# Optimization experiments

Hardware: AMD Instinct MI355X
Metric: run time of the kernel (lower is better)

## Reference

```python
import jax, jax.numpy as jnp
import numpy as np

GRID_DIMS = (64, 64, 64)
GRID_LOWER = np.array([0.0, 0.0, 0.0], np.float32)
GRID_STEPS = np.array([0.015625, 0.015625, 0.015625], np.float32)
RADIUS = 0.03125
STENCIL = 2  # ceil(radius / step)


def _poly6(d2, h):
    # standard SPH poly6 smoothing kernel: 315/(64 pi h^9) (h^2 - d^2)^3, d <= h
    c = np.float32(315.0 / (64.0 * np.pi * h ** 9))
    return jnp.where(d2 <= h * h, c * (h * h - d2) ** 3, 0.0)


def particles2grid(locs, data, density):
    # locs [B,N,3], data [B,N,C], density [B,N] -> grid [B,X,Y,Z,C]
    B, N, _ = locs.shape
    C = data.shape[-1]
    X, Y, Z = GRID_DIMS
    dims = jnp.array(GRID_DIMS, jnp.int32)
    r = jnp.arange(-STENCIL, STENCIL + 1)
    offs = jnp.stack(jnp.meshgrid(r, r, r, indexing='ij'), -1).reshape(-1, 3)  # [K,3]
    base = jnp.floor((locs - GRID_LOWER) / GRID_STEPS).astype(jnp.int32)        # [B,N,3]
    cells = base[:, :, None, :] + offs                                          # [B,N,K,3]
    centers = GRID_LOWER + (cells.astype(locs.dtype) + 0.5) * GRID_STEPS
    d2 = jnp.sum((centers - locs[:, :, None, :]) ** 2, -1)                      # [B,N,K]
    w = _poly6(d2, RADIUS)
    w = jnp.where(jnp.all((cells >= 0) & (cells < dims), -1), w, 0.0)
    contrib = w[..., None] * (data / density[..., None])[:, :, None, :]         # [B,N,K,C]
    cells = jnp.clip(cells, 0, dims - 1)
    flat = (cells[..., 0] * Y + cells[..., 1]) * Z + cells[..., 2]              # [B,N,K]

    def splat(f, c):
        return jnp.zeros((X * Y * Z, C), data.dtype).at[f.reshape(-1)].add(c.reshape(-1, C))

    return jax.vmap(splat)(flat, contrib).reshape(B, X, Y, Z, C)


def grid2particles(grid, locs):
    # trilinear interpolation of grid [B,X,Y,Z,C] at particle locations [B,N,3]
    B, X, Y, Z, C = grid.shape
    dims = jnp.array([X, Y, Z], jnp.int32)
    pos = (locs - GRID_LOWER) / GRID_STEPS - 0.5                                # cell-center coords
    i0 = jnp.floor(pos).astype(jnp.int32)
    frac = pos - i0.astype(locs.dtype)
    gflat = grid.reshape(B, X * Y * Z, C)
    gather = jax.vmap(lambda g, f: g[f])                                        # [B,N] -> [B,N,C]
    out = jnp.zeros((B, locs.shape[1], C), grid.dtype)
    for dx in (0, 1):
        for dy in (0, 1):
            for dz in (0, 1):
                off = jnp.array([dx, dy, dz], jnp.int32)
                idx = i0 + off
                wd = jnp.where(off == 1, frac, 1.0 - frac)                      # [B,N,3]
                w = wd[..., 0] * wd[..., 1] * wd[..., 2]
                w = jnp.where(jnp.all((idx >= 0) & (idx < dims), -1), w, 0.0)
                idx = jnp.clip(idx, 0, dims - 1)
                flat = (idx[..., 0] * Y + idx[..., 1]) * Z + idx[..., 2]
                out = out + w[..., None] * gather(gflat, flat)
    return out


def conv3d(x, w, b):
    y = jax.lax.conv_general_dilated(x, w, (1, 1, 1), 'SAME',
                                     dimension_numbers=('NCDHW', 'OIDHW', 'NCDHW'))
    return y + b[None, :, None, None, None]


def prelu(x, a):
    return jnp.where(x >= 0, x, a * x)


def setup_inputs() -> dict:
    key = jax.random.key(0)
    ks = jax.random.split(key, 8)
    B, N = 2, 32768
    Cin, K, Cout = 4, 32, 4
    s = lambda fan: np.float32(1.0 / np.sqrt(fan * 27))
    return {
        'locs': jax.random.uniform(ks[0], (B, N, 3), jnp.float32),
        'data': jax.random.normal(ks[1], (B, N, Cin), jnp.float32),
        'density': jax.random.uniform(ks[2], (B, N), jnp.float32, 0.5, 1.5),
        'W0': jax.random.normal(ks[3], (K, Cin, 3, 3, 3), jnp.float32) * s(Cin),
        'b0': jnp.zeros((K,), jnp.float32),
        'W1': jax.random.normal(ks[4], (K, K, 3, 3, 3), jnp.float32) * s(K),
        'b1': jnp.zeros((K,), jnp.float32),
        'W2': jax.random.normal(ks[5], (K, K, 3, 3, 3), jnp.float32) * s(K),
        'b2': jnp.zeros((K,), jnp.float32),
        'W3': jax.random.normal(ks[6], (Cout, K, 3, 3, 3), jnp.float32) * s(K),
        'b3': jnp.zeros((Cout,), jnp.float32),
        'a0': jnp.full((1,), 0.25, jnp.float32),
        'a1': jnp.full((1,), 0.25, jnp.float32),
        'a2': jnp.full((1,), 0.25, jnp.float32),
    }


def reference(locs, data, density, W0, b0, W1, b1, W2, b2, W3, b3, a0, a1, a2):
    grid = particles2grid(locs, data, density)            # [B,X,Y,Z,Cin]
    g = jnp.transpose(grid, (0, 4, 1, 2, 3))              # NCDHW
    g = prelu(conv3d(g, W0, b0), a0)
    g = prelu(conv3d(g, W1, b1), a1)
    g = prelu(conv3d(g, W2, b2), a2)
    g = conv3d(g, W3, b3)
    g = jnp.transpose(g, (0, 2, 3, 4, 1))                 # [B,X,Y,Z,Cout]
    return grid2particles(g, locs)                        # [B,N,Cout]
```

## Files before the change

kernel.cpp:

```cpp
#include <hip/hip_runtime.h>

#define BATCH 2
#define NPART 32768
#define GD 64
#define NVOX (BATCH * GD * GD * GD)

typedef unsigned short ushortT;
typedef __attribute__((ext_vector_type(8))) short short8;
typedef __attribute__((ext_vector_type(16))) float float16;

__device__ __forceinline__ float poly6_c() {
    const double H9 = 1.0 / 35184372088832.0;
    return (float)(315.0 / (64.0 * 3.14159265358979323846 * H9));
}

__device__ __forceinline__ ushortT bf16_rne(float f) {
    unsigned int u = __float_as_uint(f);
    u = (u + 0x7fffu + ((u >> 16) & 1u)) >> 16;
    return (ushortT)u;
}

__device__ __forceinline__ int imax(int a, int b) { return a > b ? a : b; }
__device__ __forceinline__ int imin(int a, int b) { return a < b ? a : b; }

__global__ void zero_ints_kernel(int* __restrict__ p, int n) {
    int t = blockIdx.x * blockDim.x + threadIdx.x;
    if (t < n) p[t] = 0;
}

__global__ void zero_borders_kernel(ushortT* __restrict__ g8,
                                    ushortT* __restrict__ gA,
                                    ushortT* __restrict__ gB) {
    int t = blockIdx.x * 256 + threadIdx.x;
    if (t >= 147456) return;
    ushortT* base; int idx;
    if (t < 16384)      { base = g8; idx = t; }
    else if (t < 81920) { base = gA; idx = t - 16384; }
    else                { base = gB; idx = t - 81920; }
    int slot = (idx & 1) * 65; idx >>= 1;
    short8 z8 = {0, 0, 0, 0, 0, 0, 0, 0};
    *(short8*)(base + ((size_t)idx * 66 + slot) * 8) = z8;
}

__global__ __launch_bounds__(256) void bin_count_kernel(
    const float* __restrict__ locs, int* __restrict__ counts) {
    int t = blockIdx.x * blockDim.x + threadIdx.x;
    if (t >= BATCH * NPART) return;
    int b = t >> 15;
    int bx = ((int)floorf(locs[t * 3 + 0] * 64.0f)) >> 1;
    int by = ((int)floorf(locs[t * 3 + 1] * 64.0f)) >> 1;
    int bz = ((int)floorf(locs[t * 3 + 2] * 64.0f)) >> 1;
    atomicAdd(&counts[b * 32768 + ((bx * 32) + by) * 32 + bz], 1);
}

__global__ __launch_bounds__(256) void scanA_kernel(
    const int* __restrict__ counts, int* __restrict__ offsets,
    int* __restrict__ blockSum) {
    __shared__ int sh[256];
    int tid = threadIdx.x, g = blockIdx.x;
    int v = counts[g * 256 + tid];
    sh[tid] = v;
    __syncthreads();
    for (int off = 1; off < 256; off <<= 1) {
        int u = (tid >= off) ? sh[tid - off] : 0;
        __syncthreads();
        sh[tid] += u;
        __syncthreads();
    }
    offsets[g * 256 + tid] = sh[tid] - v;
    if (tid == 255) blockSum[g] = sh[255];
}

__global__ __launch_bounds__(256) void scanB_kernel(
    int* __restrict__ offsets, const int* __restrict__ blockSum) {
    __shared__ int sh[256];
    int tid = threadIdx.x, g = blockIdx.x;
    sh[tid] = (tid < g) ? blockSum[tid] : 0;
    __syncthreads();
    for (int off = 128; off > 0; off >>= 1) {
        if (tid < off) sh[tid] += sh[tid + off];
        __syncthreads();
    }
    offsets[g * 256 + tid] += sh[0];
    if (g == 255 && tid == 255) offsets[65536] = BATCH * NPART;
}

__global__ __launch_bounds__(256) void bin_scatter_kernel(
    const float* __restrict__ locs, const float* __restrict__ data,
    const float* __restrict__ density, const int* __restrict__ offsets,
    int* __restrict__ cursor, float* __restrict__ payload) {
    int t = blockIdx.x * blockDim.x + threadIdx.x;
    if (t >= BATCH * NPART) return;
    int b = t >> 15;
    float px = locs[t * 3 + 0];
    float py = locs[t * 3 + 1];
    float pz = locs[t * 3 + 2];
    int bx = ((int)floorf(px * 64.0f)) >> 1;
    int by = ((int)floorf(py * 64.0f)) >> 1;
    int bz = ((int)floorf(pz * 64.0f)) >> 1;
    int bb = b * 32768 + ((bx * 32) + by) * 32 + bz;
    int slot = atomicAdd(&cursor[bb], 1);
    int idx = offsets[bb] + slot;
    float inv_d = 1.0f / density[t];
    float4 p0 = {px, py, pz, data[t * 4 + 0] * inv_d};
    float4 p1 = {data[t * 4 + 1] * inv_d, data[t * 4 + 2] * inv_d,
                 data[t * 4 + 3] * inv_d, 0.f};
    *(float4*)(payload + idx * 8)     = p0;
    *(float4*)(payload + idx * 8 + 4) = p1;
}

__global__ __launch_bounds__(256) void splat_gather_kernel(
    const float* __restrict__ payload, const int* __restrict__ offsets,
    ushortT* __restrict__ g8) {
    __shared__ float plist[256 * 8];
    __shared__ int segS[36];
    __shared__ int segP[37];
    __shared__ int shTot[1];

    int wg = blockIdx.x;
    int sb = wg & 511, b = wg >> 9;
    int X0 = (sb >> 6) * 8, Y0 = ((sb >> 3) & 7) * 8, Z0 = (sb & 7) * 8;
    int tid = threadIdx.x;

    int bxlo = imax(0, (X0 - 2) >> 1), bxhi = imin(31, (X0 + 9) >> 1);
    int bylo = imax(0, (Y0 - 2) >> 1), byhi = imin(31, (Y0 + 9) >> 1);
    int bzlo = imax(0, (Z0 - 2) >> 1), bzhi = imin(31, (Z0 + 9) >> 1);
    int ny = byhi - bylo + 1;
    int ns = (bxhi - bxlo + 1) * ny;
    if (tid < ns) {
        int bx = bxlo + tid / ny, by = bylo + tid % ny;
        int row = b * 32768 + (bx * 32 + by) * 32;
        int s = offsets[row + bzlo];
        int e = offsets[row + bzhi + 1];
        segS[tid] = s;
        segP[tid] = e - s;
    }
    __syncthreads();
    if (tid == 0) {
        int p = 0;
        for (int k = 0; k < ns; ++k) { int len = segP[k]; segP[k] = p; p += len; }
        segP[ns] = p;
        shTot[0] = p;
    }
    __syncthreads();

    const float step = 0.015625f;
    const float h2 = 0.03125f * 0.03125f;
    const float cc = poly6_c();
    int total = shTot[0];

    int l = tid & 63, w = tid >> 6;
    int cx = X0 + 4 * (w >> 1) + (l >> 4);
    int cy = Y0 + 4 * (w & 1) + ((l >> 2) & 3);
    int cz0 = Z0 + (l & 3);
    float xc  = ((float)cx  + 0.5f) * step;
    float yc  = ((float)cy  + 0.5f) * step;
    float zc0 = ((float)cz0 + 0.5f) * step;
    float zc1 = zc0 + 4.0f * step;

    float a00 = 0.f, a01 = 0.f, a02 = 0.f, a03 = 0.f;
    float a10 = 0.f, a11 = 0.f, a12 = 0.f, a13 = 0.f;

    int nchunks = (total + 255) >> 8;
    for (int ch = 0; ch < nchunks; ++ch) {
        __syncthreads();
        int jj = (ch << 8) + tid;
        if (jj < total) {
            int k = 0;
            while (jj >= segP[k + 1]) ++k;
            int idx = segS[k] + (jj - segP[k]);
            *(float4*)(plist + tid * 8)     = *(const float4*)(payload + idx * 8);
            *(float4*)(plist + tid * 8 + 4) = *(const float4*)(payload + idx * 8 + 4);
        }
        __syncthreads();
        int cnt = imin(256, total - (ch << 8));
        for (int p = 0; p < cnt; ++p) {
            float4 pa = *(const float4*)(plist + p * 8);
            float dx = pa.x - xc, dy = pa.y - yc;
            float dxy2 = fmaf(dy, dy, dx * dx);
            if (!__any(dxy2 <= h2)) continue;
            float4 pv = *(const float4*)(plist + p * 8 + 4);
            float dz0 = pa.z - zc0;
            float d20 = fmaf(dz0, dz0, dxy2);
            float u0 = fmaxf(h2 - d20, 0.f);
            float w0 = (cc * u0) * (u0 * u0);
            a00 = fmaf(w0, pa.w, a00);
            a01 = fmaf(w0, pv.x, a01);
            a02 = fmaf(w0, pv.y, a02);
            a03 = fmaf(w0, pv.z, a03);
            float dz1 = pa.z - zc1;
            float d21 = fmaf(dz1, dz1, dxy2);
            float u1 = fmaxf(h2 - d21, 0.f);
            float w1 = (cc * u1) * (u1 * u1);
            a10 = fmaf(w1, pa.w, a10);
            a11 = fmaf(w1, pv.x, a11);
            a12 = fmaf(w1, pv.y, a12);
            a13 = fmaf(w1, pv.z, a13);
        }
    }

    size_t colIdx = (size_t)(((b * 64 + cx) * 64) + cy);
    short8 o;
    o[0] = (short)bf16_rne(a00); o[1] = (short)bf16_rne(a01);
    o[2] = (short)bf16_rne(a02); o[3] = (short)bf16_rne(a03);
    o[4] = 0; o[5] = 0; o[6] = 0; o[7] = 0;
    *(short8*)(g8 + (colIdx * 66 + (cz0 + 1)) * 8) = o;
    o[0] = (short)bf16_rne(a10); o[1] = (short)bf16_rne(a11);
    o[2] = (short)bf16_rne(a12); o[3] = (short)bf16_rne(a13);
    *(short8*)(g8 + (colIdx * 66 + (cz0 + 5)) * 8) = o;
}

__global__ void repack_all_kernel(
    const float* __restrict__ W0, const float* __restrict__ W1,
    const float* __restrict__ W2, const float* __restrict__ W3,
    short* __restrict__ Bp) {
    int t = blockIdx.x * blockDim.x + threadIdx.x;
    if (t >= 176 * 512) return;
    int kt = t >> 9;
    int l = (t >> 3) & 63, j = t & 7;
    int n = l & 31, q = l >> 5;
    float v = 0.f;
    if (kt < 14) {
        int k = kt * 16 + 8 * q + j;
        int tap = k / 8, ic = k - tap * 8;
        if (tap < 27 && ic < 4) v = W0[(n * 4 + ic) * 27 + tap];
    } else {
        int rem = kt - 14;
        const float* W; int O;
        if (rem < 54)       { W = W1; O = 32; }
        else if (rem < 108) { W = W2; O = 32; rem -= 54; }
        else                { W = W3; O = 4;  rem -= 108; }
        int p = rem / 27, tap = rem - p * 27;
        int ic = p * 16 + q * 8 + j;
        if (n < O) v = W[(n * 32 + ic) * 27 + tap];
    }
    Bp[t] = (short)bf16_rne(v);
}

template <int ICG, int KT, bool FINAL>
__global__ __launch_bounds__(256) void mfma_conv_kernel(
    const ushortT* __restrict__ in, const short* __restrict__ Bpack,
    const float* __restrict__ bias, const float* __restrict__ alpha,
    const ushortT* __restrict__ zg, void* __restrict__ outv) {
    constexpr int CST = ICG * 528;
    int wg = ((blockIdx.x & 7) << 8) | (blockIdx.x >> 3);
    int zh = wg & 1, yq = (wg >> 1) & 15, xp = (wg >> 5) & 31, b = wg >> 10;
    int X0 = xp * 2, Y0 = yq * 4, Z0 = zh * 32;
    int tid = threadIdx.x;
    int l = tid & 63, w = tid >> 6;
    int wx = w >> 1, cyl = (w & 1) * 2;
    int n = l & 31, q = l >> 5;

    const ushortT* inb = in + (size_t)b * 4096 * CST;
    int Xc = X0 + wx - 1;
    int YcA = Y0 + cyl - 1;
    const ushortT* cornA = inb + (ptrdiff_t)(Xc * 64 + YcA) * CST;
    const ushortT* cornB = cornA + CST;
    int laneOff = (Z0 + (l & 31)) * 8 + ((ICG == 4) ? q * 528 : 0);

    float bval = FINAL ? (n < 4 ? bias[n] : 0.f) : bias[n];
    float16 accA, accB;
#pragma unroll
    for (int r = 0; r < 16; ++r) { accA[r] = bval; accB[r] = bval; }

    const short* bp = Bpack + (size_t)l * 8;

    auto loadAB = [&](int kt, short8& aA, short8& aB) {
        if constexpr (ICG == 4) {
            int p = kt / 27, t = kt - p * 27;
            int dx = t / 9, rr = t - dx * 9, dy = rr / 3, dz = rr - dy * 3;
            int K = (dx * 64 + dy) * CST + p * 1056 + dz * 8;
            bool xv = (unsigned)(Xc + dx) < 64u;
            bool vA = xv && (unsigned)(YcA + dy) < 64u;
            bool vB = xv && (unsigned)(YcA + 1 + dy) < 64u;
            const ushortT* bA = vA ? cornA + K : zg;
            const ushortT* bB = vB ? cornB + K : zg;
            aA = *(const short8*)(bA + laneOff);
            aB = *(const short8*)(bB + laneOff);
        } else {
            int t0 = kt * 2;
            int t1 = (kt * 2 + 1 > 26) ? 26 : kt * 2 + 1;
            int dx0 = t0 / 9, r0 = t0 - dx0 * 9, dy0 = r0 / 3, dz0 = r0 - dy0 * 3;
            int dx1 = t1 / 9, r1 = t1 - dx1 * 9, dy1 = r1 / 3, dz1 = r1 - dy1 * 3;
            int K0 = (dx0 * 64 + dy0) * CST + dz0 * 8;
            int K1 = (dx1 * 64 + dy1) * CST + dz1 * 8;
            bool v0A = (unsigned)(Xc + dx0) < 64u && (unsigned)(YcA + dy0) < 64u;
            bool v1A = (unsigned)(Xc + dx1) < 64u && (unsigned)(YcA + dy1) < 64u;
            bool v0B = (unsigned)(Xc + dx0) < 64u && (unsigned)(YcA + 1 + dy0) < 64u;
            bool v1B = (unsigned)(Xc + dx1) < 64u && (unsigned)(YcA + 1 + dy1) < 64u;
            const ushortT* a0 = v0A ? cornA + K0 : zg;
            const ushortT* a1 = v1A ? cornA + K1 : zg;
            const ushortT* b0 = v0B ? cornB + K0 : zg;
            const ushortT* b1 = v1B ? cornB + K1 : zg;
            const ushortT* sA = q ? a1 : a0;
            const ushortT* sB = q ? b1 : b0;
            aA = *(const short8*)(sA + laneOff);
            aB = *(const short8*)(sB + laneOff);
        }
    };

    short8 bf[4], fA[4], fB[4];
#pragma unroll
    for (int i = 0; i < 4; ++i) {
        bf[i] = *(const short8*)(bp + i * 512);
        loadAB(i, fA[i], fB[i]);
    }

#pragma unroll
    for (int kt = 0; kt < KT; ++kt) {
        short8 bcur = bf[kt & 3];
        short8 aA = fA[kt & 3];
        short8 aB = fB[kt & 3];
        if (kt + 4 < KT) {
            bf[kt & 3] = *(const short8*)(bp + (kt + 4) * 512);
            loadAB(kt + 4, fA[kt & 3], fB[kt & 3]);
        }
        accA = __builtin_amdgcn_mfma_f32_32x32x16_bf16(aA, bcur, accA, 0, 0, 0);
        accB = __builtin_amdgcn_mfma_f32_32x32x16_bf16(aB, bcur, accB, 0, 0, 0);
    }

    if (FINAL) {
        float* out = (float*)outv;
        size_t baseA = (size_t)(((b * 64 + X0 + wx) * 64 + (Y0 + cyl)) * 64) + Z0;
        size_t baseB = baseA + 64;
        if (n < 4) {
#pragma unroll
            for (int r = 0; r < 16; ++r) {
                int z = (r & 3) + 8 * (r >> 2) + 4 * q;
                out[(baseA + z) * 4 + n] = accA[r];
                out[(baseB + z) * 4 + n] = accB[r];
            }
        }
    } else {
        float a = alpha[0];
        ushortT* out = (ushortT*)outv;
        size_t colA = (size_t)((b * 64 + X0 + wx) * 64 + (Y0 + cyl));
        ushortT* oA = out + colA * 2112 + (size_t)(n >> 3) * 528 + (n & 7);
        ushortT* oB = oA + 2112;
#pragma unroll
        for (int r = 0; r < 16; ++r) {
            int z = (r & 3) + 8 * (r >> 2) + 4 * q;
            int zs = (Z0 + z + 1) * 8;
            float vA = accA[r];
            vA = vA >= 0.f ? vA : a * vA;
            oA[zs] = bf16_rne(vA);
            float vB = accB[r];
            vB = vB >= 0.f ? vB : a * vB;
            oB[zs] = bf16_rne(vB);
        }
    }
}

__global__ __launch_bounds__(256) void gather_kernel(
    const float* __restrict__ grid, const float* __restrict__ locs,
    float* __restrict__ out) {
    int t = blockIdx.x * blockDim.x + threadIdx.x;
    if (t >= BATCH * NPART) return;
    int b = t >> 15;

    float px = locs[t * 3 + 0] * 64.0f - 0.5f;
    float py = locs[t * 3 + 1] * 64.0f - 0.5f;
    float pz = locs[t * 3 + 2] * 64.0f - 0.5f;
    int ix = (int)floorf(px);
    int iy = (int)floorf(py);
    int iz = (int)floorf(pz);
    float fx = px - (float)ix;
    float fy = py - (float)iy;
    float fz = pz - (float)iz;

    const float* gb = grid + (size_t)b * GD * GD * GD * 4;
    float o0 = 0.f, o1 = 0.f, o2 = 0.f, o3 = 0.f;

#pragma unroll
    for (int dx = 0; dx < 2; ++dx) {
        int x = ix + dx;
        if ((unsigned)x > 63u) continue;
        float wx = dx ? fx : 1.0f - fx;
#pragma unroll
        for (int dy = 0; dy < 2; ++dy) {
            int y = iy + dy;
            if ((unsigned)y > 63u) continue;
            float wy = dy ? fy : 1.0f - fy;
#pragma unroll
            for (int dz = 0; dz < 2; ++dz) {
                int z = iz + dz;
                if ((unsigned)z > 63u) continue;
                float wz = dz ? fz : 1.0f - fz;
                float w = wx * wy * wz;
                const float4 g = *(const float4*)(gb + (size_t)(((x * GD) + y) * GD + z) * 4);
                o0 += w * g.x; o1 += w * g.y; o2 += w * g.z; o3 += w * g.w;
            }
        }
    }
    out[t * 4 + 0] = o0;
    out[t * 4 + 1] = o1;
    out[t * 4 + 2] = o2;
    out[t * 4 + 3] = o3;
}

extern "C" void kernel_launch(void* const* d_in, const int* in_sizes, int n_in,
                              void* d_out, int out_size, void* d_ws, size_t ws_size,
                              hipStream_t stream) {
    const float* locs    = (const float*)d_in[0];
    const float* data    = (const float*)d_in[1];
    const float* density = (const float*)d_in[2];
    const float* W0 = (const float*)d_in[3];
    const float* b0 = (const float*)d_in[4];
    const float* W1 = (const float*)d_in[5];
    const float* b1 = (const float*)d_in[6];
    const float* W2 = (const float*)d_in[7];
    const float* b2 = (const float*)d_in[8];
    const float* W3 = (const float*)d_in[9];
    const float* b3 = (const float*)d_in[10];
    const float* a0 = (const float*)d_in[11];
    const float* a1 = (const float*)d_in[12];
    const float* a2 = (const float*)d_in[13];
    float* out = (float*)d_out;

    char* ws = (char*)d_ws;
    ushortT* g8  = (ushortT*)(ws);
    ushortT* gA  = (ushortT*)(ws + 8650752);
    ushortT* gB  = (ushortT*)(ws + 43253760);
    float*  gF   = (float*)(ws + 77856768);
    short*  Bp   = (short*)(ws + 86245376);
    short*  Bp0  = Bp;
    short*  Bp1  = Bp + 14 * 512;
    short*  Bp2  = Bp + 68 * 512;
    short*  Bp3  = Bp + 122 * 512;
    ushortT* zguard = (ushortT*)(ws + 86425600);
    int*   counts   = (int*)(ws + 86429824);
    int*   cursor   = (int*)(ws + 86691968);
    int*   offsets  = (int*)(ws + 86954112);
    int*   blockSum = (int*)(ws + 87216384);
    float* payload  = (float*)(ws + 87217408);

    zero_ints_kernel<<<(132128 + 255) / 256, 256, 0, stream>>>((int*)zguard, 132128);
    zero_borders_kernel<<<576, 256, 0, stream>>>(g8, gA, gB);
    bin_count_kernel<<<(BATCH * NPART) / 256, 256, 0, stream>>>(locs, counts);
    scanA_kernel<<<256, 256, 0, stream>>>(counts, offsets, blockSum);
    scanB_kernel<<<256, 256, 0, stream>>>(offsets, blockSum);
    bin_scatter_kernel<<<(BATCH * NPART) / 256, 256, 0, stream>>>(
        locs, data, density, offsets, cursor, payload);

    repack_all_kernel<<<(176 * 512 + 255) / 256, 256, 0, stream>>>(W0, W1, W2, W3, Bp);

    splat_gather_kernel<<<BATCH * 512, 256, 0, stream>>>(payload, offsets, g8);

    const int CGRID = 2048;
    mfma_conv_kernel< 1, 14, false><<<CGRID, 256, 0, stream>>>(g8, Bp0, b0, a0, zguard, gA);
    mfma_conv_kernel< 4, 54, false><<<CGRID, 256, 0, stream>>>(gA, Bp1, b1, a1, zguard, gB);
    mfma_conv_kernel< 4, 54, false><<<CGRID, 256, 0, stream>>>(gB, Bp2, b2, a2, zguard, gA);
    mfma_conv_kernel< 4, 54, true ><<<CGRID, 256, 0, stream>>>(gA, Bp3, b3, b3, zguard, gF);

    gather_kernel<<<(BATCH * NPART) / 256, 256, 0, stream>>>(gF, locs, out);
}
```

Baseline: 269.1 us.

## Register-tile four y-outputs per wave in 32-channel conv to reuse A fragments

The 32-channel conv layers are restructured so each wave computes four consecutive y output columns over a full 32-wide z span. Each loaded input fragment along y is reused across up to three filter taps, which cuts redundant global loads per MFMA. The grid is halved to 1024 blocks, and the software-pipelined prefetch of the old kernel is removed. The trade-off is four accumulators per wave (more registers, lower occupancy) and less explicit latency hiding. The first layer becomes its own non-pipelined kernel.

Result: slower. 308.0 us (+14.5%).

```diff
diff --git a/kernel.cpp b/kernel.cpp
--- a/kernel.cpp
+++ b/kernel.cpp
@@ -237,12 +237,11 @@
     Bp[t] = (short)bf16_rne(v);
 }
 
-template <int ICG, int KT, bool FINAL>
-__global__ __launch_bounds__(256) void mfma_conv_kernel(
+__global__ __launch_bounds__(256) void mfma_conv1_kernel(
     const ushortT* __restrict__ in, const short* __restrict__ Bpack,
     const float* __restrict__ bias, const float* __restrict__ alpha,
-    const ushortT* __restrict__ zg, void* __restrict__ outv) {
-    constexpr int CST = ICG * 528;
+    const ushortT* __restrict__ zg, ushortT* __restrict__ out) {
+    constexpr int CST = 528;
     int wg = ((blockIdx.x & 7) << 8) | (blockIdx.x >> 3);
     int zh = wg & 1, yq = (wg >> 1) & 15, xp = (wg >> 5) & 31, b = wg >> 10;
     int X0 = xp * 2, Y0 = yq * 4, Z0 = zh * 32;
@@ -256,97 +255,149 @@
     int YcA = Y0 + cyl - 1;
     const ushortT* cornA = inb + (ptrdiff_t)(Xc * 64 + YcA) * CST;
     const ushortT* cornB = cornA + CST;
-    int laneOff = (Z0 + (l & 31)) * 8 + ((ICG == 4) ? q * 528 : 0);
-
-    float bval = FINAL ? (n < 4 ? bias[n] : 0.f) : bias[n];
+    int laneOff = (Z0 + (l & 31)) * 8;
+
+    float bval = bias[n];
     float16 accA, accB;
 #pragma unroll
     for (int r = 0; r < 16; ++r) { accA[r] = bval; accB[r] = bval; }
 
     const short* bp = Bpack + (size_t)l * 8;
 
-    auto loadAB = [&](int kt, short8& aA, short8& aB) {
-        if constexpr (ICG == 4) {
-            int p = kt / 27, t = kt - p * 27;
-            int dx = t / 9, rr = t - dx * 9, dy = rr / 3, dz = rr - dy * 3;
-            int K = (dx * 64 + dy) * CST + p * 1056 + dz * 8;
-            bool xv = (unsigned)(Xc + dx) < 64u;
-            bool vA = xv && (unsigned)(YcA + dy) < 64u;
-            bool vB = xv && (unsigned)(YcA + 1 + dy) < 64u;
-            const ushortT* bA = vA ? cornA + K : zg;
-            const ushortT* bB = vB ? cornB + K : zg;
-            aA = *(const short8*)(bA + laneOff);
-            aB = *(const short8*)(bB + laneOff);
-        } else {
-            int t0 = kt * 2;
-            int t1 = (kt * 2 + 1 > 26) ? 26 : kt * 2 + 1;
-            int dx0 = t0 / 9, r0 = t0 - dx0 * 9, dy0 = r0 / 3, dz0 = r0 - dy0 * 3;
-            int dx1 = t1 / 9, r1 = t1 - dx1 * 9, dy1 = r1 / 3, dz1 = r1 - dy1 * 3;
-            int K0 = (dx0 * 64 + dy0) * CST + dz0 * 8;
-            int K1 = (dx1 * 64 + dy1) * CST + dz1 * 8;
-            bool v0A = (unsigned)(Xc + dx0) < 64u && (unsigned)(YcA + dy0) < 64u;
-            bool v1A = (unsigned)(Xc + dx1) < 64u && (unsigned)(YcA + dy1) < 64u;
-            bool v0B = (unsigned)(Xc + dx0) < 64u && (unsigned)(YcA + 1 + dy0) < 64u;
-            bool v1B = (unsigned)(Xc + dx1) < 64u && (unsigned)(YcA + 1 + dy1) < 64u;
-            const ushortT* a0 = v0A ? cornA + K0 : zg;
-            const ushortT* a1 = v1A ? cornA + K1 : zg;
-            const ushortT* b0 = v0B ? cornB + K0 : zg;
-            const ushortT* b1 = v1B ? cornB + K1 : zg;
-            const ushortT* sA = q ? a1 : a0;
-            const ushortT* sB = q ? b1 : b0;
-            aA = *(const short8*)(sA + laneOff);
-            aB = *(const short8*)(sB + laneOff);
-        }
-    };
-
-    short8 bf[4], fA[4], fB[4];
-#pragma unroll
-    for (int i = 0; i < 4; ++i) {
-        bf[i] = *(const short8*)(bp + i * 512);
-        loadAB(i, fA[i], fB[i]);
-    }
-
-#pragma unroll
-    for (int kt = 0; kt < KT; ++kt) {
-        short8 bcur = bf[kt & 3];
-        short8 aA = fA[kt & 3];
-        short8 aB = fB[kt & 3];
-        if (kt + 4 < KT) {
-            bf[kt & 3] = *(const short8*)(bp + (kt + 4) * 512);
-            loadAB(kt + 4, fA[kt & 3], fB[kt & 3]);
-        }
+#pragma unroll
+    for (int kt = 0; kt < 14; ++kt) {
+        short8 bcur = *(const short8*)(bp + kt * 512);
+        int t0 = kt * 2;
+        int t1 = (kt * 2 + 1 > 26) ? 26 : kt * 2 + 1;
+        int dx0 = t0 / 9, r0 = t0 - dx0 * 9, dy0 = r0 / 3, dz0 = r0 - dy0 * 3;
+        int dx1 = t1 / 9, r1 = t1 - dx1 * 9, dy1 = r1 / 3, dz1 = r1 - dy1 * 3;
+        int K0 = (dx0 * 64 + dy0) * CST + dz0 * 8;
+        int K1 = (dx1 * 64 + dy1) * CST + dz1 * 8;
+        bool v0A = (unsigned)(Xc + dx0) < 64u && (unsigned)(YcA + dy0) < 64u;
+        bool v1A = (unsigned)(Xc + dx1) < 64u && (unsigned)(YcA + dy1) < 64u;
+        bool v0B = (unsigned)(Xc + dx0) < 64u && (unsigned)(YcA + 1 + dy0) < 64u;
+        bool v1B = (unsigned)(Xc + dx1) < 64u && (unsigned)(YcA + 1 + dy1) < 64u;
+        const ushortT* a0 = v0A ? cornA + K0 : zg;
+        const ushortT* a1 = v1A ? cornA + K1 : zg;
+        const ushortT* b0 = v0B ? cornB + K0 : zg;
+        const ushortT* b1 = v1B ? cornB + K1 : zg;
+        const ushortT* sA = q ? a1 : a0;
+        const ushortT* sB = q ? b1 : b0;
+        short8 aA = *(const short8*)(sA + laneOff);
+        short8 aB = *(const short8*)(sB + laneOff);
         accA = __builtin_amdgcn_mfma_f32_32x32x16_bf16(aA, bcur, accA, 0, 0, 0);
         accB = __builtin_amdgcn_mfma_f32_32x32x16_bf16(aB, bcur, accB, 0, 0, 0);
     }
 
+    float a = alpha[0];
+    size_t colA = (size_t)((b * 64 + X0 + wx) * 64 + (Y0 + cyl));
+    ushortT* oA = out + colA * 2112 + (size_t)(n >> 3) * 528 + (n & 7);
+    ushortT* oB = oA + 2112;
+#pragma unroll
+    for (int r = 0; r < 16; ++r) {
+        int z = (r & 3) + 8 * (r >> 2) + 4 * q;
+        int zs = (Z0 + z + 1) * 8;
+        float vA = accA[r];
+        vA = vA >= 0.f ? vA : a * vA;
+        oA[zs] = bf16_rne(vA);
+        float vB = accB[r];
+        vB = vB >= 0.f ? vB : a * vB;
+        oB[zs] = bf16_rne(vB);
+    }
+}
+
+template <bool FINAL>
+__global__ __launch_bounds__(256) void mfma_conv4_kernel(
+    const ushortT* __restrict__ in, const short* __restrict__ Bpack,
+    const float* __restrict__ bias, const float* __restrict__ alpha,
+    const ushortT* __restrict__ zg, void* __restrict__ outv) {
+    constexpr int CST = 4 * 528;
+    int wg = ((blockIdx.x & 7) << 7) | (blockIdx.x >> 3);
+    int yq = wg & 15, xp = (wg >> 4) & 31, b = wg >> 9;
+    int X0 = xp * 2, Y0 = yq * 4;
+    int tid = threadIdx.x;
+    int l = tid & 63, w = tid >> 6;
+    int wx = w >> 1, zh = w & 1;
+    int Z0 = zh * 32;
+    int n = l & 31, q = l >> 5;
+
+    const ushortT* inb = in + (size_t)b * 4096 * CST;
+    int Xc = X0 + wx - 1;
+    int Yc = Y0 - 1;
+
+    float bval = FINAL ? (n < 4 ? bias[n] : 0.f) : bias[n];
+    float16 acc[4];
+#pragma unroll
+    for (int o = 0; o < 4; ++o)
+#pragma unroll
+        for (int r = 0; r < 16; ++r) acc[o][r] = bval;
+
+    const short* bp = Bpack + (size_t)l * 8;
+    int laneZ = (Z0 + (l & 31)) * 8 + q * 528;
+
+#pragma unroll
+    for (int p = 0; p < 2; ++p) {
+#pragma unroll
+        for (int dx = 0; dx < 3; ++dx) {
+            bool xv = (unsigned)(Xc + dx) < 64u;
+            const ushortT* colB[6];
+#pragma unroll
+            for (int yc = 0; yc < 6; ++yc) {
+                bool yv = (unsigned)(Yc + yc) < 64u;
+                colB[yc] = (xv && yv)
+                    ? inb + (ptrdiff_t)((Xc + dx) * 64 + (Yc + yc)) * CST
+                    : zg;
+            }
+#pragma unroll
+            for (int dz = 0; dz < 3; ++dz) {
+                int lo = laneZ + dz * 8 + p * 1056;
+                short8 Bf[3];
+#pragma unroll
+                for (int ty = 0; ty < 3; ++ty)
+                    Bf[ty] = *(const short8*)(bp +
+                        (size_t)(p * 27 + dx * 9 + ty * 3 + dz) * 512);
+#pragma unroll
+                for (int yc = 0; yc < 6; ++yc) {
+                    short8 A = *(const short8*)(colB[yc] + lo);
+#pragma unroll
+                    for (int ty = 0; ty < 3; ++ty) {
+                        int yo = yc - ty;
+                        if (yo >= 0 && yo <= 3)
+                            acc[yo] = __builtin_amdgcn_mfma_f32_32x32x16_bf16(
+                                A, Bf[ty], acc[yo], 0, 0, 0);
+                    }
+                }
+            }
+        }
+    }
+
     if (FINAL) {
         float* out = (float*)outv;
-        size_t baseA = (size_t)(((b * 64 + X0 + wx) * 64 + (Y0 + cyl)) * 64) + Z0;
-        size_t baseB = baseA + 64;
         if (n < 4) {
 #pragma unroll
-            for (int r = 0; r < 16; ++r) {
-                int z = (r & 3) + 8 * (r >> 2) + 4 * q;
-                out[(baseA + z) * 4 + n] = accA[r];
-                out[(baseB + z) * 4 + n] = accB[r];
+            for (int o = 0; o < 4; ++o) {
+                size_t base = (size_t)(((b * 64 + X0 + wx) * 64 + (Y0 + o)) * 64) + Z0;
+#pragma unroll
+                for (int r = 0; r < 16; ++r) {
+                    int z = (r & 3) + 8 * (r >> 2) + 4 * q;
+                    out[(base + z) * 4 + n] = acc[o][r];
+                }
             }
         }
     } else {
         float a = alpha[0];
         ushortT* out = (ushortT*)outv;
-        size_t colA = (size_t)((b * 64 + X0 + wx) * 64 + (Y0 + cyl));
-        ushortT* oA = out + colA * 2112 + (size_t)(n >> 3) * 528 + (n & 7);
-        ushortT* oB = oA + 2112;
-#pragma unroll
-        for (int r = 0; r < 16; ++r) {
-            int z = (r & 3) + 8 * (r >> 2) + 4 * q;
-            int zs = (Z0 + z + 1) * 8;
-            float vA = accA[r];
-            vA = vA >= 0.f ? vA : a * vA;
-            oA[zs] = bf16_rne(vA);
-            float vB = accB[r];
-            vB = vB >= 0.f ? vB : a * vB;
-            oB[zs] = bf16_rne(vB);
+#pragma unroll
+        for (int o = 0; o < 4; ++o) {
+            size_t col = (size_t)((b * 64 + X0 + wx) * 64 + (Y0 + o));
+            ushortT* op = out + col * 2112 + (size_t)(n >> 3) * 528 + (n & 7);
+#pragma unroll
+            for (int r = 0; r < 16; ++r) {
+                int z = (r & 3) + 8 * (r >> 2) + 4 * q;
+                float v = acc[o][r];
+                v = v >= 0.f ? v : a * v;
+                op[(Z0 + z + 1) * 8] = bf16_rne(v);
+            }
         }
     }
 }
@@ -446,11 +497,10 @@
 
     splat_gather_kernel<<<BATCH * 512, 256, 0, stream>>>(payload, offsets, g8);
 
-    const int CGRID = 2048;
-    mfma_conv_kernel< 1, 14, false><<<CGRID, 256, 0, stream>>>(g8, Bp0, b0, a0, zguard, gA);
-    mfma_conv_kernel< 4, 54, false><<<CGRID, 256, 0, stream>>>(gA, Bp1, b1, a1, zguard, gB);
-    mfma_conv_kernel< 4, 54, false><<<CGRID, 256, 0, stream>>>(gB, Bp2, b2, a2, zguard, gA);
-    mfma_conv_kernel< 4, 54, true ><<<CGRID, 256, 0, stream>>>(gA, Bp3, b3, b3, zguard, gF);
+    mfma_conv1_kernel<<<2048, 256, 0, stream>>>(g8, Bp0, b0, a0, zguard, gA);
+    mfma_conv4_kernel<false><<<1024, 256, 0, stream>>>(gA, Bp1, b1, a1, zguard, gB);
+    mfma_conv4_kernel<false><<<1024, 256, 0, stream>>>(gB, Bp2, b2, a2, zguard, gA);
+    mfma_conv4_kernel<true ><<<1024, 256, 0, stream>>>(gA, Bp3, b3, b3, zguard, gF);
 
     gather_kernel<<<(BATCH * NPART) / 256, 256, 0, stream>>>(gF, locs, out);
 }
```
